# Kernel tuning notes

Hardware: AMD Instinct MI355X
Metric: run time of the kernel (lower is better)

## Reference

```python
import jax, jax.numpy as jnp
import numpy as np

B, S, D = 4, 1024, 1024
E, F, TOPK = 16, 512, 4


def setup_inputs() -> dict:
    key = jax.random.key(0)
    k1, k2, k3, k4, k5 = jax.random.split(key, 5)
    scale = 0.02
    return {
        "x": jax.random.normal(k1, (B, S, D), dtype=jnp.float32),
        "Wr": jax.random.normal(k2, (D, E), dtype=jnp.float32) * scale,   # router
        "Wg": jax.random.normal(k3, (E, D, F), dtype=jnp.float32) * scale,  # gate proj
        "Wu": jax.random.normal(k4, (E, D, F), dtype=jnp.float32) * scale,  # up proj
        "Wd": jax.random.normal(k5, (E, F, D), dtype=jnp.float32) * scale,  # down proj
    }


def reference(x, Wr, Wg, Wu, Wd):
    b, s, d = x.shape
    xf = x.reshape(-1, d)                      # [N, D], N = B*S
    n = xf.shape[0]
    e = Wr.shape[1]

    # --- router: softmax over experts, top-k, renormalized weights ---
    probs = jax.nn.softmax(xf @ Wr, axis=-1)   # [N, E]
    w, idx = jax.lax.top_k(probs, TOPK)        # [N, K], [N, K]
    w = w / jnp.sum(w, axis=-1, keepdims=True)

    # combine weights per (token, expert); zero for unselected experts.
    # Equivalent to the per-expert where/gather/scatter-add loop in torch.
    cw = jnp.zeros((n, e), dtype=xf.dtype).at[jnp.arange(n)[:, None], idx].add(w)

    # --- per-expert gated FFN (SwiGLU), combined with routing weights ---
    def body(acc, ws):
        wg, wu, wd, c = ws                     # [D,F], [D,F], [F,D], [N]
        h = jax.nn.silu(xf @ wg) * (xf @ wu)   # [N, F]
        return acc + c[:, None] * (h @ wd), None

    out, _ = jax.lax.scan(body, jnp.zeros_like(xf), (Wg, Wu, Wd, cw.T))
    return out.reshape(b, s, d)
```

## Files before the change

kernel.cpp:

```cpp
#include <hip/hip_runtime.h>

#define N_TOK 4096
#define DIM   1024
#define NE    16
#define NF    512
#define TOPK  4
#define CAP   4096
#define NPAIR (N_TOK * TOPK)
#define MAXTILES 144

typedef _Float16 v8h __attribute__((ext_vector_type(8)));
typedef float    v4f __attribute__((ext_vector_type(4)));

__global__ __launch_bounds__(64) void router_kernel(
    const float* __restrict__ x, const float* __restrict__ Wr,
    int* __restrict__ tokIdx, float* __restrict__ tokW,
    unsigned short* __restrict__ xb)
{
    int t = blockIdx.x;
    int l = threadIdx.x;
    double z[NE];
#pragma unroll
    for (int e = 0; e < NE; e++) z[e] = 0.0;
    const float* xrow = x + (size_t)t * DIM;
#pragma unroll
    for (int i = 0; i < 16; i++) {
        int d = i * 64 + l;
        double xv = (double)xrow[d];
        const float4* wr = (const float4*)(Wr + d * NE);
        float4 w0 = wr[0], w1 = wr[1], w2 = wr[2], w3 = wr[3];
        z[0]  += xv * w0.x; z[1]  += xv * w0.y; z[2]  += xv * w0.z; z[3]  += xv * w0.w;
        z[4]  += xv * w1.x; z[5]  += xv * w1.y; z[6]  += xv * w1.z; z[7]  += xv * w1.w;
        z[8]  += xv * w2.x; z[9]  += xv * w2.y; z[10] += xv * w2.z; z[11] += xv * w2.w;
        z[12] += xv * w3.x; z[13] += xv * w3.y; z[14] += xv * w3.z; z[15] += xv * w3.w;
    }
    const float4* xv4 = (const float4*)xrow;
#pragma unroll
    for (int h2 = 0; h2 < 2; h2++) {
        int base = h2 * 512 + l * 8;
        float4 a = xv4[h2 * 128 + l * 2];
        float4 b = xv4[h2 * 128 + l * 2 + 1];
        union { unsigned short u[8]; uint4 v; } p;
        p.u[0] = __builtin_bit_cast(unsigned short, (_Float16)a.x);
        p.u[1] = __builtin_bit_cast(unsigned short, (_Float16)a.y);
        p.u[2] = __builtin_bit_cast(unsigned short, (_Float16)a.z);
        p.u[3] = __builtin_bit_cast(unsigned short, (_Float16)a.w);
        p.u[4] = __builtin_bit_cast(unsigned short, (_Float16)b.x);
        p.u[5] = __builtin_bit_cast(unsigned short, (_Float16)b.y);
        p.u[6] = __builtin_bit_cast(unsigned short, (_Float16)b.z);
        p.u[7] = __builtin_bit_cast(unsigned short, (_Float16)b.w);
        *(uint4*)(xb + (size_t)t * DIM + base) = p.v;
    }
#pragma unroll
    for (int e = 0; e < NE; e++) {
#pragma unroll
        for (int m = 1; m < 64; m <<= 1) z[e] += __shfl_xor(z[e], m, 64);
    }
    if (l == 0) {
        bool taken[NE];
#pragma unroll
        for (int e = 0; e < NE; e++) taken[e] = false;
        int idx[TOPK]; double sel[TOPK];
        for (int k = 0; k < TOPK; k++) {
            int bi = 0; double bv = -1.0e300;
            for (int e = 0; e < NE; e++)
                if (!taken[e] && z[e] > bv) { bv = z[e]; bi = e; }
            taken[bi] = true; idx[k] = bi; sel[k] = bv;
        }
        double m = sel[0];
        double ex[TOPK]; double s = 0.0;
        for (int k = 0; k < TOPK; k++) { ex[k] = exp(sel[k] - m); s += ex[k]; }
        for (int k = 0; k < TOPK; k++) {
            tokIdx[t * TOPK + k] = idx[k];
            tokW[t * TOPK + k]   = (float)(ex[k] / s);
        }
    }
}

__global__ __launch_bounds__(256) void bin_kernel(
    const int* __restrict__ tokIdx,
    int* __restrict__ cnt, int* __restrict__ bpair)
{
    int e = blockIdx.x;
    int tid = threadIdx.x, lane = tid & 63, wv = tid >> 6;
    __shared__ int wsum[4];
    __shared__ int sbase;
    if (tid == 0) sbase = 0;
    __syncthreads();
    unsigned long long lt = (1ULL << lane) - 1ULL;
#pragma unroll 1
    for (int c0 = 0; c0 < NPAIR; c0 += 1024) {
        int i0 = c0 + tid * 4;
        int4 v = *(const int4*)(tokIdx + i0);
        int m[4] = {v.x == e, v.y == e, v.z == e, v.w == e};
        int r[4]; int wcnt = 0;
#pragma unroll
        for (int j = 0; j < 4; j++) {
            unsigned long long bal = __ballot(m[j] != 0);
            r[j] = wcnt + __popcll(bal & lt);
            wcnt += __popcll(bal);
        }
        if (lane == 0) wsum[wv] = wcnt;
        __syncthreads();
        int woff = sbase;
        for (int k = 0; k < wv; k++) woff += wsum[k];
#pragma unroll
        for (int j = 0; j < 4; j++)
            if (m[j]) bpair[e * CAP + woff + r[j]] = i0 + j;
        __syncthreads();
        if (tid == 0) sbase += wsum[0] + wsum[1] + wsum[2] + wsum[3];
        __syncthreads();
    }
    if (tid == 0) cnt[e] = sbase;
}

__global__ __launch_bounds__(256) void prep_weight_kernel(
    const float* __restrict__ Wg, const float* __restrict__ Wu,
    const float* __restrict__ Wd,
    unsigned short* __restrict__ Wg_t, unsigned short* __restrict__ Wu_t,
    unsigned short* __restrict__ Wd_t)
{
    int z = blockIdx.y;
    int which = z >> 4, e = z & 15;
    const float* src; unsigned short* dst; int R, C, RIL;
    if (which == 0)      { src = Wg; dst = Wg_t; R = DIM; C = NF;  RIL = 6; }
    else if (which == 1) { src = Wu; dst = Wu_t; R = DIM; C = NF;  RIL = 6; }
    else                 { src = Wd; dst = Wd_t; R = NF;  C = DIM; RIL = 7; }
    int bx = blockIdx.x;
    int cbl, rbl;
    if (which < 2) { cbl = bx & 7;  rbl = bx >> 3; }
    else           { cbl = bx & 15; rbl = bx >> 4; }
    int c0 = cbl * 64, r0 = rbl * 64;

    __shared__ float tile[64][65];
    const float* s = src + (size_t)e * R * C;
    int t = threadIdx.x;
    int tr = t >> 4, tc = (t & 15) * 4;
#pragma unroll
    for (int i = 0; i < 4; i++) {
        int row = i * 16 + tr;
        float4 v = *(const float4*)(s + (size_t)(r0 + row) * C + c0 + tc);
        tile[row][tc + 0] = v.x; tile[row][tc + 1] = v.y;
        tile[row][tc + 2] = v.z; tile[row][tc + 3] = v.w;
    }
    __syncthreads();
    int ktPerE = R >> 5;
    int cbPerE = C >> RIL;
    int imgSz  = (1 << RIL) * 32;
#pragma unroll
    for (int i = 0; i < 4; i++) {
        int nr = i * 16 + tr;
        int orow = c0 + nr;
        int k0 = r0 + tc;
        int cb = orow >> RIL;
        int r  = orow & ((1 << RIL) - 1);
        int kt = k0 >> 5;
        size_t off = ((size_t)(e * cbPerE + cb) * ktPerE + kt) * imgSz
                   + r * 32 + (k0 & 31);
        union { unsigned short u[4]; uint2 v; } p;
#pragma unroll
        for (int j = 0; j < 4; j++)
            p.u[j] = __builtin_bit_cast(unsigned short, (_Float16)tile[tc + j][nr]);
        *(uint2*)(dst + off) = p.v;
    }
}

__device__ __forceinline__ int ldsw(int row, int chunk) {
    return row * 32 + (chunk ^ ((row >> 1) & 3)) * 8;
}

__device__ __forceinline__ void gload16(const unsigned short* g, unsigned short* l) {
    __builtin_amdgcn_global_load_lds(
        (const __attribute__((address_space(1))) void*)g,
        (__attribute__((address_space(3))) void*)l, 16, 0, 0);
}

__device__ __forceinline__ bool find_tile(const int* __restrict__ cnt,
                                          int ti, int& e, int& mt, int& tbase) {
    int rt = 0;
#pragma unroll 1
    for (int ee = 0; ee < NE; ee++) {
        int nt = (cnt[ee] + 127) >> 7;
        if (ti < rt + nt) { e = ee; mt = ti - rt; tbase = rt; return true; }
        rt += nt;
    }
    return false;
}

__global__ __launch_bounds__(256) void ffn_gate_up_kernel(
    const unsigned short* __restrict__ xb,
    const unsigned short* __restrict__ Wg_t,
    const unsigned short* __restrict__ Wu_t,
    const int* __restrict__ cnt,
    const int* __restrict__ bpair,
    unsigned short* __restrict__ h_t)
{
    int fb = blockIdx.x, ti = blockIdx.y;
    int e, mt, tbase;
    if (!find_tile(cnt, ti, e, mt, tbase)) return;
    int count = cnt[e];

    __shared__ __align__(16) unsigned short sX[2 * 128 * 32];
    __shared__ __align__(16) unsigned short sG[2 * 64 * 32];
    __shared__ __align__(16) unsigned short sU[2 * 64 * 32];
    __shared__ int sTok[128];

    int tid = threadIdx.x, lane = tid & 63, w = tid >> 6;
    if (tid < 128) {
        int pos = mt * 128 + tid;
        sTok[tid] = bpair[e * CAP + min(pos, count - 1)] >> 2;
    }
    __syncthreads();

    int srow0 = w * 16 + (lane >> 2);
    int srow1 = srow0 + 64;
    int spos  = lane & 3;
    int cx0 = spos ^ ((srow0 >> 1) & 3);
    int cx1 = spos ^ ((srow1 >> 1) & 3);
    const unsigned short* gX0 = xb + (size_t)sTok[srow0] * DIM + cx0 * 8;
    const unsigned short* gX1 = xb + (size_t)sTok[srow1] * DIM + cx1 * 8;
    const unsigned short* gG  = Wg_t + ((size_t)(e * 8 + fb) * 32) * 2048 + srow0 * 32 + cx0 * 8;
    const unsigned short* gU  = Wu_t + ((size_t)(e * 8 + fb) * 32) * 2048 + srow0 * 32 + cx0 * 8;
    unsigned short* dX0 = sX + (size_t)(w * 16) * 32;
    unsigned short* dX1 = sX + (size_t)(64 + w * 16) * 32;
    unsigned short* dG  = sG + (size_t)(w * 16) * 32;
    unsigned short* dU  = sU + (size_t)(w * 16) * 32;

    int row = lane & 15, q = lane >> 4;
    int rw = w & 1, cw = w >> 1;
    int aoff[4], goff[2];
#pragma unroll
    for (int mi = 0; mi < 4; mi++) aoff[mi] = ldsw(rw * 64 + mi * 16 + row, q);
#pragma unroll
    for (int ni = 0; ni < 2; ni++) goff[ni] = ldsw(cw * 32 + ni * 16 + row, q);

    v4f accG[4][2], accU[4][2];
    v4f zero = {0.f, 0.f, 0.f, 0.f};
#pragma unroll
    for (int mi = 0; mi < 4; mi++)
#pragma unroll
        for (int ni = 0; ni < 2; ni++) { accG[mi][ni] = zero; accU[mi][ni] = zero; }

#define STAGE_GU(b, kt) do {                                   \
        gload16(gX0 + (kt) * 32, dX0 + (b) * 4096);            \
        gload16(gX1 + (kt) * 32, dX1 + (b) * 4096);            \
        gload16(gG + (size_t)(kt) * 2048, dG + (b) * 2048);    \
        gload16(gU + (size_t)(kt) * 2048, dU + (b) * 2048);    \
    } while (0)

    STAGE_GU(0, 0);
    __syncthreads();

#pragma unroll 1
    for (int kt = 0; kt < 32; kt++) {
        int buf = kt & 1;
        if (kt < 31) STAGE_GU(buf ^ 1, kt + 1);
        const unsigned short* bX = sX + buf * 4096;
        const unsigned short* bGp = sG + buf * 2048;
        const unsigned short* bUp = sU + buf * 2048;
        v8h a[4], bg[2], bu[2];
#pragma unroll
        for (int mi = 0; mi < 4; mi++) a[mi] = *(const v8h*)&bX[aoff[mi]];
#pragma unroll
        for (int ni = 0; ni < 2; ni++) {
            bg[ni] = *(const v8h*)&bGp[goff[ni]];
            bu[ni] = *(const v8h*)&bUp[goff[ni]];
        }
#pragma unroll
        for (int mi = 0; mi < 4; mi++)
#pragma unroll
            for (int ni = 0; ni < 2; ni++) {
                accG[mi][ni] = __builtin_amdgcn_mfma_f32_16x16x32_f16(a[mi], bg[ni], accG[mi][ni], 0, 0, 0);
                accU[mi][ni] = __builtin_amdgcn_mfma_f32_16x16x32_f16(a[mi], bu[ni], accU[mi][ni], 0, 0, 0);
            }
        __syncthreads();
    }
#undef STAGE_GU

    size_t himg = (size_t)(tbase + mt) * 16;
#pragma unroll
    for (int mi = 0; mi < 4; mi++)
#pragma unroll
        for (int ni = 0; ni < 2; ni++) {
            int f = fb * 64 + cw * 32 + ni * 16 + row;
#pragma unroll
            for (int i = 0; i < 4; i++) {
                int rl = rw * 64 + mi * 16 + q * 4 + i;
                int pos = mt * 128 + rl;
                if (pos < count) {
                    float gv = accG[mi][ni][i];
                    float uv = accU[mi][ni][i];
                    float hv = gv * uv / (1.0f + __expf(-gv));
                    size_t off = (himg + (f >> 5)) * 4096 + rl * 32 + (f & 31);
                    h_t[off] = __builtin_bit_cast(unsigned short, (_Float16)hv);
                }
            }
        }
}

__global__ __launch_bounds__(256) void ffn_down_kernel(
    const unsigned short* __restrict__ h_t,
    const unsigned short* __restrict__ Wd_t,
    const int* __restrict__ cnt,
    const int* __restrict__ bpair,
    unsigned short* __restrict__ part)
{
    int ti = blockIdx.x, db = blockIdx.y;
    int e, mt, tbase;
    if (!find_tile(cnt, ti, e, mt, tbase)) return;
    int count = cnt[e];

    __shared__ __align__(16) unsigned short sH[2 * 128 * 32];
    __shared__ __align__(16) unsigned short sW[2 * 128 * 32];
    __shared__ int sPair[128];

    int tid = threadIdx.x, lane = tid & 63, w = tid >> 6;
    if (tid < 128) {
        int pos = mt * 128 + tid;
        sPair[tid] = bpair[e * CAP + min(pos, count - 1)];
    }
    __syncthreads();

    int srow0 = w * 16 + (lane >> 2);
    int srow1 = srow0 + 64;
    int spos  = lane & 3;
    int c0 = spos ^ ((srow0 >> 1) & 3);
    int c1 = spos ^ ((srow1 >> 1) & 3);
    const unsigned short* hbase = h_t + ((size_t)(tbase + mt) * 16) * 4096;
    const unsigned short* wbase = Wd_t + ((size_t)(e * 8 + db) * 16) * 4096;
    const unsigned short* gH0 = hbase + srow0 * 32 + c0 * 8;
    const unsigned short* gH1 = hbase + srow1 * 32 + c1 * 8;
    const unsigned short* gW0 = wbase + srow0 * 32 + c0 * 8;
    const unsigned short* gW1 = wbase + srow1 * 32 + c1 * 8;
    unsigned short* dH0 = sH + (size_t)(w * 16) * 32;
    unsigned short* dH1 = sH + (size_t)(64 + w * 16) * 32;
    unsigned short* dW0 = sW + (size_t)(w * 16) * 32;
    unsigned short* dW1 = sW + (size_t)(64 + w * 16) * 32;

    int row = lane & 15, q = lane >> 4;
    int rw = w & 1, cw = w >> 1;
    int aoff[4], boff[4];
#pragma unroll
    for (int mi = 0; mi < 4; mi++) aoff[mi] = ldsw(rw * 64 + mi * 16 + row, q);
#pragma unroll
    for (int ni = 0; ni < 4; ni++) boff[ni] = ldsw(cw * 64 + ni * 16 + row, q);

    v4f acc[4][4];
    v4f zero = {0.f, 0.f, 0.f, 0.f};
#pragma unroll
    for (int mi = 0; mi < 4; mi++)
#pragma unroll
        for (int ni = 0; ni < 4; ni++) acc[mi][ni] = zero;

#define STAGE_D(b, kt) do {                                         \
        gload16(gH0 + (size_t)(kt) * 4096, dH0 + (b) * 4096);       \
        gload16(gH1 + (size_t)(kt) * 4096, dH1 + (b) * 4096);       \
        gload16(gW0 + (size_t)(kt) * 4096, dW0 + (b) * 4096);       \
        gload16(gW1 + (size_t)(kt) * 4096, dW1 + (b) * 4096);       \
    } while (0)

    STAGE_D(0, 0);
    __syncthreads();

#pragma unroll 1
    for (int kt = 0; kt < 16; kt++) {
        int buf = kt & 1;
        if (kt < 15) STAGE_D(buf ^ 1, kt + 1);
        const unsigned short* bH = sH + buf * 4096;
        const unsigned short* bW = sW + buf * 4096;
        v8h a[4], b[4];
#pragma unroll
        for (int mi = 0; mi < 4; mi++) a[mi] = *(const v8h*)&bH[aoff[mi]];
#pragma unroll
        for (int ni = 0; ni < 4; ni++) b[ni] = *(const v8h*)&bW[boff[ni]];
#pragma unroll
        for (int mi = 0; mi < 4; mi++)
#pragma unroll
            for (int ni = 0; ni < 4; ni++)
                acc[mi][ni] = __builtin_amdgcn_mfma_f32_16x16x32_f16(a[mi], b[ni], acc[mi][ni], 0, 0, 0);
        __syncthreads();
    }
#undef STAGE_D

#pragma unroll
    for (int mi = 0; mi < 4; mi++)
#pragma unroll
        for (int ni = 0; ni < 4; ni++) {
            int col = db * 128 + cw * 64 + ni * 16 + row;
#pragma unroll
            for (int i = 0; i < 4; i++) {
                int rl = rw * 64 + mi * 16 + q * 4 + i;
                int pos = mt * 128 + rl;
                if (pos < count) {
                    int p = sPair[rl];
                    part[(size_t)p * DIM + col] =
                        __builtin_bit_cast(unsigned short, (_Float16)acc[mi][ni][i]);
                }
            }
        }
}

__global__ __launch_bounds__(256) void combine_kernel(
    const unsigned short* __restrict__ part, const float* __restrict__ tokW,
    float* __restrict__ out)
{
    int gid = blockIdx.x * 256 + threadIdx.x;
    int t = gid >> 8;
    int c = (gid & 255) * 4;
    float4 r = {0.f, 0.f, 0.f, 0.f};
#pragma unroll
    for (int k = 0; k < TOPK; k++) {
        float wk = tokW[t * TOPK + k];
        union { uint2 u; _Float16 h[4]; } cv;
        cv.u = *(const uint2*)(part + ((size_t)(t * TOPK + k)) * DIM + c);
        r.x += wk * (float)cv.h[0];
        r.y += wk * (float)cv.h[1];
        r.z += wk * (float)cv.h[2];
        r.w += wk * (float)cv.h[3];
    }
    *(float4*)(out + (size_t)t * DIM + c) = r;
}

extern "C" void kernel_launch(void* const* d_in, const int* in_sizes, int n_in,
                              void* d_out, int out_size, void* d_ws, size_t ws_size,
                              hipStream_t stream)
{
    const float* x  = (const float*)d_in[0];
    const float* Wr = (const float*)d_in[1];
    const float* Wg = (const float*)d_in[2];
    const float* Wu = (const float*)d_in[3];
    const float* Wd = (const float*)d_in[4];
    float* out = (float*)d_out;
    char* ws = (char*)d_ws;

    size_t off = 0;
    int* tokIdx = (int*)(ws + off);   off += (size_t)NPAIR * 4;
    float* tokW = (float*)(ws + off); off += (size_t)NPAIR * 4;
    int* cnt    = (int*)(ws + off);   off += 256;
    int* bpair  = (int*)(ws + off);   off += (size_t)NE * CAP * 4;
    unsigned short* xb   = (unsigned short*)(ws + off); off += (size_t)N_TOK * DIM * 2;
    unsigned short* Wg_t = (unsigned short*)(ws + off); off += (size_t)NE * DIM * NF * 2;
    unsigned short* Wu_t = (unsigned short*)(ws + off); off += (size_t)NE * DIM * NF * 2;
    unsigned short* Wd_t = (unsigned short*)(ws + off); off += (size_t)NE * DIM * NF * 2;
    unsigned short* h_t  = (unsigned short*)(ws + off); off += (size_t)MAXTILES * 16 * 4096 * 2;
    unsigned short* part = (unsigned short*)(ws + off); off += (size_t)NPAIR * DIM * 2;

    router_kernel<<<N_TOK, 64, 0, stream>>>(x, Wr, tokIdx, tokW, xb);
    bin_kernel<<<NE, 256, 0, stream>>>(tokIdx, cnt, bpair);
    prep_weight_kernel<<<dim3(128, 48), 256, 0, stream>>>(Wg, Wu, Wd, Wg_t, Wu_t, Wd_t);
    ffn_gate_up_kernel<<<dim3(8, MAXTILES), 256, 0, stream>>>(
        xb, Wg_t, Wu_t, cnt, bpair, h_t);
    ffn_down_kernel<<<dim3(MAXTILES, 8), 256, 0, stream>>>(
        h_t, Wd_t, cnt, bpair, part);
    combine_kernel<<<(N_TOK * DIM) / (256 * 4), 256, 0, stream>>>(part, tokW, out);
}
```

Baseline: 294.5 us.

## Merge weight-prep blocks into router and gate/up kernels to overlap work

```diff
diff --git a/kernel.cpp b/kernel.cpp
--- a/kernel.cpp
+++ b/kernel.cpp
@@ -8,17 +8,72 @@
 #define CAP   4096
 #define NPAIR (N_TOK * TOPK)
 #define MAXTILES 144
+#define GU_BLOCKS (8 * MAXTILES)
+#define PREPD_BLOCKS (NE * 128)
 
 typedef _Float16 v8h __attribute__((ext_vector_type(8)));
 typedef float    v4f __attribute__((ext_vector_type(4)));
 
-__global__ __launch_bounds__(64) void router_kernel(
+__device__ __forceinline__ void prep_tile(
+    const float* __restrict__ src, unsigned short* __restrict__ dst,
+    int R, int C, int RIL, int e, int cbl, int rbl, float (*tile)[65])
+{
+    int c0 = cbl * 64, r0 = rbl * 64;
+    const float* s = src + (size_t)e * R * C;
+    int t = threadIdx.x;
+    int tr = t >> 4, tc = (t & 15) * 4;
+#pragma unroll
+    for (int i = 0; i < 4; i++) {
+        int row = i * 16 + tr;
+        float4 v = *(const float4*)(s + (size_t)(r0 + row) * C + c0 + tc);
+        tile[row][tc + 0] = v.x; tile[row][tc + 1] = v.y;
+        tile[row][tc + 2] = v.z; tile[row][tc + 3] = v.w;
+    }
+    __syncthreads();
+    int ktPerE = R >> 5;
+    int cbPerE = C >> RIL;
+    int imgSz  = (1 << RIL) * 32;
+#pragma unroll
+    for (int i = 0; i < 4; i++) {
+        int nr = i * 16 + tr;
+        int orow = c0 + nr;
+        int k0 = r0 + tc;
+        int cb = orow >> RIL;
+        int r  = orow & ((1 << RIL) - 1);
+        int kt = k0 >> 5;
+        size_t off = ((size_t)(e * cbPerE + cb) * ktPerE + kt) * imgSz
+                   + r * 32 + (k0 & 31);
+        union { unsigned short u[4]; uint2 v; } p;
+#pragma unroll
+        for (int j = 0; j < 4; j++)
+            p.u[j] = __builtin_bit_cast(unsigned short, (_Float16)tile[tc + j][nr]);
+        *(uint2*)(dst + off) = p.v;
+    }
+}
+
+__global__ __launch_bounds__(256) void router_prep_kernel(
     const float* __restrict__ x, const float* __restrict__ Wr,
+    const float* __restrict__ Wg, const float* __restrict__ Wu,
     int* __restrict__ tokIdx, float* __restrict__ tokW,
-    unsigned short* __restrict__ xb)
-{
-    int t = blockIdx.x;
-    int l = threadIdx.x;
+    unsigned short* __restrict__ xb,
+    unsigned short* __restrict__ Wg_t, unsigned short* __restrict__ Wu_t)
+{
+    __shared__ __align__(16) float tile[64][65];
+    int bid = blockIdx.x;
+    if (bid >= 1024) {
+        int pid = bid - 1024;
+        int z = pid >> 7;
+        int which = z >> 4, e = z & 15;
+        int bx = pid & 127;
+        int cbl = bx & 7, rbl = bx >> 3;
+        prep_tile(which ? Wu : Wg, which ? Wu_t : Wg_t,
+                  DIM, NF, 6, e, cbl, rbl, tile);
+        return;
+    }
+    int tid = threadIdx.x;
+    int w = tid >> 6, l = tid & 63;
+    int t = bid * 4 + w;
+
     double z[NE];
 #pragma unroll
     for (int e = 0; e < NE; e++) z[e] = 0.0;
@@ -114,57 +169,6 @@
     if (tid == 0) cnt[e] = sbase;
 }
 
-__global__ __launch_bounds__(256) void prep_weight_kernel(
-    const float* __restrict__ Wg, const float* __restrict__ Wu,
-    const float* __restrict__ Wd,
-    unsigned short* __restrict__ Wg_t, unsigned short* __restrict__ Wu_t,
-    unsigned short* __restrict__ Wd_t)
-{
-    int z = blockIdx.y;
-    int which = z >> 4, e = z & 15;
-    const float* src; unsigned short* dst; int R, C, RIL;
-    if (which == 0)      { src = Wg; dst = Wg_t; R = DIM; C = NF;  RIL = 6; }
-    else if (which == 1) { src = Wu; dst = Wu_t; R = DIM; C = NF;  RIL = 6; }
-    else                 { src = Wd; dst = Wd_t; R = NF;  C = DIM; RIL = 7; }
-    int bx = blockIdx.x;
-    int cbl, rbl;
-    if (which < 2) { cbl = bx & 7;  rbl = bx >> 3; }
-    else           { cbl = bx & 15; rbl = bx >> 4; }
-    int c0 = cbl * 64, r0 = rbl * 64;
-
-    __shared__ float tile[64][65];
-    const float* s = src + (size_t)e * R * C;
-    int t = threadIdx.x;
-    int tr = t >> 4, tc = (t & 15) * 4;
-#pragma unroll
-    for (int i = 0; i < 4; i++) {
-        int row = i * 16 + tr;
-        float4 v = *(const float4*)(s + (size_t)(r0 + row) * C + c0 + tc);
-        tile[row][tc + 0] = v.x; tile[row][tc + 1] = v.y;
-        tile[row][tc + 2] = v.z; tile[row][tc + 3] = v.w;
-    }
-    __syncthreads();
-    int ktPerE = R >> 5;
-    int cbPerE = C >> RIL;
-    int imgSz  = (1 << RIL) * 32;
-#pragma unroll
-    for (int i = 0; i < 4; i++) {
-        int nr = i * 16 + tr;
-        int orow = c0 + nr;
-        int k0 = r0 + tc;
-        int cb = orow >> RIL;
-        int r  = orow & ((1 << RIL) - 1);
-        int kt = k0 >> 5;
-        size_t off = ((size_t)(e * cbPerE + cb) * ktPerE + kt) * imgSz
-                   + r * 32 + (k0 & 31);
-        union { unsigned short u[4]; uint2 v; } p;
-#pragma unroll
-        for (int j = 0; j < 4; j++)
-            p.u[j] = __builtin_bit_cast(unsigned short, (_Float16)tile[tc + j][nr]);
-        *(uint2*)(dst + off) = p.v;
-    }
-}
-
 __device__ __forceinline__ int ldsw(int row, int chunk) {
     return row * 32 + (chunk ^ ((row >> 1) & 3)) * 8;
 }
@@ -193,17 +197,30 @@
     const unsigned short* __restrict__ Wu_t,
     const int* __restrict__ cnt,
     const int* __restrict__ bpair,
-    unsigned short* __restrict__ h_t)
-{
-    int fb = blockIdx.x, ti = blockIdx.y;
+    unsigned short* __restrict__ h_t,
+    const float* __restrict__ Wd,
+    unsigned short* __restrict__ Wd_t)
+{
+    __shared__ __align__(16) unsigned char smem[33536];
+    unsigned short* sX = (unsigned short*)smem;
+    unsigned short* sG = (unsigned short*)(smem + 16384);
+    unsigned short* sU = (unsigned short*)(smem + 24576);
+    int* sTok = (int*)(smem + 32768);
+    float (*tile)[65] = (float (*)[65])smem;
+
+    int bid = blockIdx.x;
+    if (bid >= GU_BLOCKS) {
+        int pid = bid - GU_BLOCKS;
+        int e = pid >> 7;
+        int bx = pid & 127;
+        int cbl = bx & 15, rbl = bx >> 4;
+        prep_tile(Wd, Wd_t, NF, DIM, 7, e, cbl, rbl, tile);
+        return;
+    }
+    int fb = bid & 7, ti = bid >> 3;
     int e, mt, tbase;
     if (!find_tile(cnt, ti, e, mt, tbase)) return;
     int count = cnt[e];
-
-    __shared__ __align__(16) unsigned short sX[2 * 128 * 32];
-    __shared__ __align__(16) unsigned short sG[2 * 64 * 32];
-    __shared__ __align__(16) unsigned short sU[2 * 64 * 32];
-    __shared__ int sTok[128];
 
     int tid = threadIdx.x, lane = tid & 63, w = tid >> 6;
     if (tid < 128) {
@@ -445,11 +462,11 @@
     unsigned short* h_t  = (unsigned short*)(ws + off); off += (size_t)MAXTILES * 16 * 4096 * 2;
     unsigned short* part = (unsigned short*)(ws + off); off += (size_t)NPAIR * DIM * 2;
 
-    router_kernel<<<N_TOK, 64, 0, stream>>>(x, Wr, tokIdx, tokW, xb);
+    router_prep_kernel<<<1024 + 4096, 256, 0, stream>>>(
+        x, Wr, Wg, Wu, tokIdx, tokW, xb, Wg_t, Wu_t);
     bin_kernel<<<NE, 256, 0, stream>>>(tokIdx, cnt, bpair);
-    prep_weight_kernel<<<dim3(128, 48), 256, 0, stream>>>(Wg, Wu, Wd, Wg_t, Wu_t, Wd_t);
-    ffn_gate_up_kernel<<<dim3(8, MAXTILES), 256, 0, stream>>>(
-        xb, Wg_t, Wu_t, cnt, bpair, h_t);
+    ffn_gate_up_kernel<<<GU_BLOCKS + PREPD_BLOCKS, 256, 0, stream>>>(
+        xb, Wg_t, Wu_t, cnt, bpair, h_t, Wd, Wd_t);
     ffn_down_kernel<<<dim3(MAXTILES, 8), 256, 0, stream>>>(
         h_t, Wd_t, cnt, bpair, part);
     combine_kernel<<<(N_TOK * DIM) / (256 * 4), 256, 0, stream>>>(part, tokW, out);
```

New measurement: 271.4 us. -7.8%, faster.
